# Kernel optimization log

Measured on AMD Instinct MI355X. Metric: run time of the kernel, lower is better.

The kernel has to match this reference:

```python
import jax, jax.numpy as jnp
import numpy as np

NHEADS = 16  # init kwarg


def setup_inputs() -> dict:
    key = jax.random.key(0)
    ks = jax.random.split(key, 3)
    S, B, E = 2048, 4, 1024
    x = jax.random.normal(ks[0], (S, B, E), dtype=jnp.float32)
    Wqkv = jax.random.normal(ks[1], (E, 3 * E), dtype=jnp.float32) * 0.02
    bqkv = jnp.zeros((3 * E,), dtype=jnp.float32)
    Wout = jax.random.normal(ks[2], (E, E), dtype=jnp.float32) * 0.02
    bout = jnp.zeros((E,), dtype=jnp.float32)
    return {"x": x, "Wqkv": Wqkv, "bqkv": bqkv, "Wout": Wout, "bout": bout}


def reference(x, Wqkv, bqkv, Wout, bout):
    S, B, E = x.shape
    H = NHEADS
    d = E // H
    scale = jnp.sqrt(jnp.asarray(E / H, dtype=x.dtype))  # sqrt(d_head)
    qkv = x @ Wqkv + bqkv                      # (S, B, 3E)
    q, k, v = jnp.split(qkv, 3, axis=-1)       # each (S, B, E)
    # (S, B, E) -> (S, B*H, d) -> (B*H, S, d), matching torch reshape+permute
    q = q.reshape(S, B * H, d).transpose(1, 0, 2)
    k = k.reshape(S, B * H, d).transpose(1, 0, 2)
    v = v.reshape(S, B * H, d).transpose(1, 0, 2)
    scores = jnp.einsum('hsd,htd->hst', q, k) / scale  # (B*H, S, S)
    attn = jax.nn.softmax(scores, axis=-1)
    o = jnp.einsum('hst,htd->hsd', attn, v)    # (B*H, S, d)
    o = o.transpose(1, 0, 2).reshape(S, B, E)  # back to (S, B, E)
    return o @ Wout + bout
```

## Files before the change

### kernel.cpp

```cpp
#include <hip/hip_runtime.h>

typedef short s16x8 __attribute__((ext_vector_type(8)));
typedef float f32x4 __attribute__((ext_vector_type(4)));
typedef float f32x16 __attribute__((ext_vector_type(16)));
typedef unsigned int u32x2 __attribute__((ext_vector_type(2)));

__device__ inline float bf2f(unsigned short u) {
    union { float f; unsigned int i; } x; x.i = ((unsigned int)u) << 16; return x.f;
}
__device__ inline unsigned short f2bf(float f) {
    union { float f; unsigned int i; } x; x.f = f;
    unsigned int r = x.i + 0x7fff + ((x.i >> 16) & 1);
    return (unsigned short)(r >> 16);
}
__device__ inline unsigned int pack_bf16(float a, float b) {
    unsigned int ia = __float_as_uint(a) + 0x8000u;
    unsigned int ib = __float_as_uint(b) + 0x8000u;
    return (ia >> 16) | (ib & 0xffff0000u);
}

__device__ inline void gload_lds16(const unsigned short* g, unsigned short* l) {
    __builtin_amdgcn_global_load_lds(
        (const __attribute__((address_space(1))) unsigned int*)g,
        (__attribute__((address_space(3))) unsigned int*)l, 16, 0, 0);
}

__global__ void detect_dtype(const unsigned short* __restrict__ x16, int* flag) {
    __shared__ int s[256];
    int tid = threadIdx.x;
    int cnt = 0;
    for (int i = tid; i < 4096; i += 256) {
        unsigned short u = x16[2 * i];
        int e = (u >> 7) & 0xFF;
        if (e >= 117 && e <= 129) cnt++;
    }
    s[tid] = cnt;
    __syncthreads();
    for (int off = 128; off; off >>= 1) {
        if (tid < off) s[tid] += s[tid + off];
        __syncthreads();
    }
    if (tid == 0) *flag = (s[0] < 2048) ? 1 : 0;
}

__global__ void convert_x(const void* __restrict__ in, unsigned short* __restrict__ out,
                          const int* __restrict__ flag, int n) {
    int mode = *flag;
    int i0 = (blockIdx.x * 256 + threadIdx.x) * 8;
    if (i0 >= n) return;
    if (mode) {
        const float* f = (const float*)in;
#pragma unroll
        for (int j = 0; j < 8; ++j) out[i0 + j] = f2bf(f[i0 + j]);
    } else {
        *(s16x8*)(out + i0) = *(const s16x8*)((const unsigned short*)in + i0);
    }
}

__global__ void cvt_bias(const void* __restrict__ in, float* __restrict__ out,
                         const int* __restrict__ flag, int n) {
    int i = blockIdx.x * 256 + threadIdx.x;
    if (i >= n) return;
    out[i] = (*flag) ? ((const float*)in)[i] : bf2f(((const unsigned short*)in)[i]);
}

__global__ void transpose_cvt(const void* __restrict__ in, unsigned short* __restrict__ out,
                              const int* __restrict__ flag, int R, int C) {
    __shared__ unsigned short t[64][72];
    int mode = *flag;
    int r0 = blockIdx.y * 64, c0 = blockIdx.x * 64;
    for (int i = threadIdx.x; i < 64 * 64; i += 256) {
        int r = i >> 6, c = i & 63;
        size_t idx = (size_t)(r0 + r) * C + (c0 + c);
        t[r][c] = mode ? f2bf(((const float*)in)[idx]) : ((const unsigned short*)in)[idx];
    }
    __syncthreads();
    for (int i = threadIdx.x; i < 64 * 64; i += 256) {
        int c = i >> 6, r = i & 63;
        out[(size_t)(c0 + c) * R + (r0 + r)] = t[r][c];
    }
}

__global__ __launch_bounds__(256) void transpose_v(
    const unsigned short* __restrict__ qkv, unsigned short* __restrict__ Vt) {
    __shared__ unsigned short t[64][72];
    int bh = blockIdx.y; int b = bh >> 4, h = bh & 15;
    int k0 = blockIdx.x * 64;
    int tid = threadIdx.x;
    int kr = tid >> 2, db = (tid & 3) * 16;
    const unsigned short* src = qkv + ((size_t)(k0 + kr) * 4 + b) * 3072 + 2048 + h * 64 + db;
    *(s16x8*)&t[kr][db] = *(const s16x8*)src;
    *(s16x8*)&t[kr][db + 8] = *(const s16x8*)(src + 8);
    __syncthreads();
    int d = tid >> 2, kb = (tid & 3) * 16;
    unsigned short* dst = Vt + (size_t)bh * 131072 + (size_t)d * 2048 + k0 + kb;
    s16x8 a, c;
#pragma unroll
    for (int j = 0; j < 8; ++j) a[j] = t[kb + j][d];
#pragma unroll
    for (int j = 0; j < 8; ++j) c[j] = t[kb + 8 + j][d];
    *(s16x8*)dst = a;
    *(s16x8*)(dst + 8) = c;
}

__global__ __launch_bounds__(512) void gemm_pipe_kernel(
    const unsigned short* __restrict__ A, const unsigned short* __restrict__ BT,
    const float* __restrict__ bias, void* __restrict__ Cout,
    int M, int N, int K, int qcols, float qscale, const int* __restrict__ outf32flag) {
    __shared__ unsigned short As[3][256 * 64];
    __shared__ unsigned short Bs[3][128 * 64];
    int tid = threadIdx.x;
    int lane = tid & 63, w = tid >> 6;
    int wr = w >> 1, wc = w & 1;
    int g = lane >> 4, qh = lane & 15;
    int m0 = blockIdx.y * 256, n0 = blockIdx.x * 128;
    int vxor = (lane & 7) ^ (lane >> 3);
    int axor = qh & 7;

    f32x4 z = {0.f, 0.f, 0.f, 0.f};
    f32x4 acc[4][4];
#pragma unroll
    for (int m = 0; m < 4; ++m)
#pragma unroll
        for (int n = 0; n < 4; ++n) acc[m][n] = z;

    const unsigned short* Asrc = A + (size_t)(m0 + w * 8 + (lane >> 3)) * K + vxor * 8;
    const unsigned short* Bsrc = BT + (size_t)(n0 + w * 8 + (lane >> 3)) * K + vxor * 8;

#define STAGE_A(buf, t, j) gload_lds16(Asrc + (size_t)(j) * 64 * K + (size_t)(t) * 64, \
                                       &As[buf][0] + (j) * 4096 + w * 512)
#define STAGE_B(buf, t, j) gload_lds16(Bsrc + (size_t)(j) * 64 * K + (size_t)(t) * 64, \
                                       &Bs[buf][0] + (j) * 4096 + w * 512)

    int NT = K >> 6;
    STAGE_A(0, 0, 0); STAGE_A(0, 0, 1); STAGE_A(0, 0, 2); STAGE_A(0, 0, 3);
    STAGE_B(0, 0, 0); STAGE_B(0, 0, 1);
    STAGE_A(1, 1, 0); STAGE_A(1, 1, 1); STAGE_A(1, 1, 2); STAGE_A(1, 1, 3);
    STAGE_B(1, 1, 0); STAGE_B(1, 1, 1);
    asm volatile("s_waitcnt vmcnt(6)" ::: "memory");
    __builtin_amdgcn_s_barrier();

    int cur = 0;
    for (int t = 0; t < NT; ++t) {
        int nx = cur + 2; if (nx >= 3) nx -= 3;
        bool pf = (t + 2) < NT;
        const unsigned short* Ab = &As[cur][0];
        const unsigned short* Bb = &Bs[cur][0];

        s16x8 bf[4][2];
#pragma unroll
        for (int n = 0; n < 4; ++n)
#pragma unroll
            for (int kk = 0; kk < 2; ++kk)
                bf[n][kk] = *(const s16x8*)(Bb + (size_t)(wc * 64 + n * 16 + qh) * 64 +
                                            (((kk * 4 + g) ^ axor) * 8));

        if (pf) { STAGE_A(nx, t + 2, 0); STAGE_A(nx, t + 2, 1); STAGE_B(nx, t + 2, 0); }
        {
            s16x8 af[2][2];
#pragma unroll
            for (int i = 0; i < 2; ++i)
#pragma unroll
                for (int kk = 0; kk < 2; ++kk)
                    af[i][kk] = *(const s16x8*)(Ab + (size_t)(wr * 64 + i * 16 + qh) * 64 +
                                                (((kk * 4 + g) ^ axor) * 8));
            __builtin_amdgcn_s_setprio(1);
#pragma unroll
            for (int kk = 0; kk < 2; ++kk)
#pragma unroll
                for (int i = 0; i < 2; ++i)
#pragma unroll
                    for (int n = 0; n < 4; ++n)
                        acc[i][n] = __builtin_amdgcn_mfma_f32_16x16x32_bf16(af[i][kk], bf[n][kk], acc[i][n], 0, 0, 0);
            __builtin_amdgcn_s_setprio(0);
        }
        __builtin_amdgcn_s_barrier();

        if (pf) { STAGE_A(nx, t + 2, 2); STAGE_A(nx, t + 2, 3); STAGE_B(nx, t + 2, 1); }
        {
            s16x8 af[2][2];
#pragma unroll
            for (int i = 0; i < 2; ++i)
#pragma unroll
                for (int kk = 0; kk < 2; ++kk)
                    af[i][kk] = *(const s16x8*)(Ab + (size_t)(wr * 64 + (i + 2) * 16 + qh) * 64 +
                                                (((kk * 4 + g) ^ axor) * 8));
            __builtin_amdgcn_s_setprio(1);
#pragma unroll
            for (int kk = 0; kk < 2; ++kk)
#pragma unroll
                for (int i = 0; i < 2; ++i)
#pragma unroll
                    for (int n = 0; n < 4; ++n)
                        acc[i + 2][n] = __builtin_amdgcn_mfma_f32_16x16x32_bf16(af[i][kk], bf[n][kk], acc[i + 2][n], 0, 0, 0);
            __builtin_amdgcn_s_setprio(0);
        }
        if (t + 1 < NT) {
            if (pf) asm volatile("s_waitcnt vmcnt(6)" ::: "memory");
            else    asm volatile("s_waitcnt vmcnt(0)" ::: "memory");
            __builtin_amdgcn_s_barrier();
        }
        cur = cur + 1; if (cur >= 3) cur -= 3;
    }
#undef STAGE_A
#undef STAGE_B

    bool f32out = (outf32flag != nullptr) && (*outf32flag != 0);
    int crow0 = m0 + wr * 64;
    int ccol0 = n0 + wc * 64;
#pragma unroll
    for (int n = 0; n < 4; ++n) {
        int col = ccol0 + n * 16 + qh;
        float bv = bias[col];
        float qs = (col < qcols) ? qscale : 1.0f;
#pragma unroll
        for (int m = 0; m < 4; ++m) {
            int rbase = crow0 + m * 16 + g * 4;
#pragma unroll
            for (int qq = 0; qq < 4; ++qq) {
                float v = (acc[m][n][qq] + bv) * qs;
                if (f32out)
                    ((float*)Cout)[(size_t)(rbase + qq) * N + col] = v;
                else
                    ((unsigned short*)Cout)[(size_t)(rbase + qq) * N + col] = f2bf(v);
            }
        }
    }
}

__global__ __launch_bounds__(256) void attn_kernel(
    const unsigned short* __restrict__ qkv, const unsigned short* __restrict__ Vt,
    unsigned short* __restrict__ O) {
    int bh = blockIdx.y;
    int b = bh >> 4, h = bh & 15;
    int q0 = blockIdx.x * 128;
    int tid = threadIdx.x, lane = tid & 63, w = tid >> 6;
    int l31 = lane & 31, l5 = lane >> 5;

    __shared__ unsigned short Ks[8 * 64 * 8];
    __shared__ unsigned short Vs[64 * 64];

    int qrow = q0 + w * 32 + l31;
    const unsigned short* qp = qkv + ((size_t)qrow * 4 + b) * 3072 + h * 64 + l5 * 8;
    s16x8 qf[4];
#pragma unroll
    for (int st = 0; st < 4; ++st) qf[st] = *(const s16x8*)(qp + st * 16);

    f32x16 z16 = {0.f,0.f,0.f,0.f,0.f,0.f,0.f,0.f,0.f,0.f,0.f,0.f,0.f,0.f,0.f,0.f};
    f32x16 oacc[2];
    oacc[0] = z16; oacc[1] = z16;
    float lrun = 0.f;

    int vxor = (lane & 7) ^ (lane >> 3);

    for (int k0 = 0; k0 < 2048; k0 += 64) {
        __syncthreads();
        {
            const unsigned short* ksrc = qkv + ((size_t)(k0 + lane) * 4 + b) * 3072 + 1024 + h * 64;
            gload_lds16(ksrc + w * 8, Ks + (size_t)w * 512);
            gload_lds16(ksrc + (w + 4) * 8, Ks + (size_t)(w + 4) * 512);
        }
#pragma unroll
        for (int c = 0; c < 2; ++c) {
            int d = (c * 4 + w) * 8 + (lane >> 3);
            const unsigned short* vsrc = Vt + (size_t)bh * 131072 + (size_t)d * 2048 + k0 + vxor * 8;
            gload_lds16(vsrc, Vs + (size_t)(c * 4 + w) * 512);
        }
        __syncthreads();

        f32x16 sc[2];
        sc[0] = z16; sc[1] = z16;
#pragma unroll
        for (int st = 0; st < 4; ++st) {
            int gd = st * 2 + l5;
#pragma unroll
            for (int kt = 0; kt < 2; ++kt) {
                s16x8 kf = *(const s16x8*)(Ks + ((size_t)(gd * 64 + kt * 32 + l31)) * 8);
                sc[kt] = __builtin_amdgcn_mfma_f32_32x32x16_bf16(kf, qf[st], sc[kt], 0, 0, 0);
            }
        }

        float rsum = 0.f;
#pragma unroll
        for (int kt = 0; kt < 2; ++kt) {
            float p[16];
#pragma unroll
            for (int r = 0; r < 16; ++r) {
                p[r] = __builtin_amdgcn_exp2f(sc[kt][r]);
                rsum += p[r];
            }
#pragma unroll
            for (int ks1 = 0; ks1 < 2; ++ks1) {
                unsigned int A0 = pack_bf16(p[8 * ks1 + 0], p[8 * ks1 + 1]);
                unsigned int A1 = pack_bf16(p[8 * ks1 + 2], p[8 * ks1 + 3]);
                unsigned int B0 = pack_bf16(p[8 * ks1 + 4], p[8 * ks1 + 5]);
                unsigned int B1 = pack_bf16(p[8 * ks1 + 6], p[8 * ks1 + 7]);
                u32x2 r0 = __builtin_amdgcn_permlane32_swap(A0, B0, false, false);
                u32x2 r1 = __builtin_amdgcn_permlane32_swap(A1, B1, false, false);
                union { unsigned int u[4]; s16x8 v; } uu;
                uu.u[0] = r0[0];
                uu.u[1] = r1[0];
                uu.u[2] = r0[1];
                uu.u[3] = r1[1];
                int ks = kt * 2 + ks1;
#pragma unroll
                for (int dt = 0; dt < 2; ++dt) {
                    int d = dt * 32 + l31;
                    int kb = (ks * 2 + l5) ^ (d & 7);
                    s16x8 vf = *(const s16x8*)(Vs + (size_t)d * 64 + kb * 8);
                    oacc[dt] = __builtin_amdgcn_mfma_f32_32x32x16_bf16(vf, uu.v, oacc[dt], 0, 0, 0);
                }
            }
        }
        rsum += __shfl_xor(rsum, 32);
        lrun += rsum;
    }

    float rl = 1.f / lrun;
    unsigned short* orow = O + ((size_t)qrow * 4 + b) * 1024 + h * 64 + l5 * 4;
#pragma unroll
    for (int dt = 0; dt < 2; ++dt) {
#pragma unroll
        for (int g2 = 0; g2 < 4; ++g2) {
            u32x2 pv;
            pv[0] = pack_bf16(oacc[dt][4 * g2 + 0] * rl, oacc[dt][4 * g2 + 1] * rl);
            pv[1] = pack_bf16(oacc[dt][4 * g2 + 2] * rl, oacc[dt][4 * g2 + 3] * rl);
            *(u32x2*)(orow + dt * 32 + g2 * 8) = pv;
        }
    }
}

extern "C" void kernel_launch(void* const* d_in, const int* in_sizes, int n_in,
                              void* d_out, int out_size, void* d_ws, size_t ws_size,
                              hipStream_t stream) {
    const void* x    = d_in[0];
    const void* Wqkv = d_in[1];
    const void* bqkv = d_in[2];
    const void* Wout = d_in[3];
    const void* bout = d_in[4];

    char* ws = (char*)d_ws;
    unsigned short* qkv   = (unsigned short*)(ws);
    unsigned short* Obuf  = (unsigned short*)(ws + 50331648);
    unsigned short* WqkvT = (unsigned short*)(ws + 67108864);
    unsigned short* WoutT = (unsigned short*)(ws + 73400320);
    unsigned short* xb    = (unsigned short*)(ws + 75497472);
    unsigned short* Vtg   = xb;
    float*          bq_f  = (float*)(ws + 92274688);
    float*          bo_f  = (float*)(ws + 92286976);
    int*            flag  = (int*)(ws + 92291072);

    detect_dtype<<<1, 256, 0, stream>>>((const unsigned short*)x, flag);
    convert_x<<<4096, 256, 0, stream>>>(x, xb, flag, 8388608);
    cvt_bias<<<12, 256, 0, stream>>>(bqkv, bq_f, flag, 3072);
    cvt_bias<<<4, 256, 0, stream>>>(bout, bo_f, flag, 1024);
    transpose_cvt<<<dim3(48, 16), 256, 0, stream>>>(Wqkv, WqkvT, flag, 1024, 3072);
    transpose_cvt<<<dim3(16, 16), 256, 0, stream>>>(Wout, WoutT, flag, 1024, 1024);

    gemm_pipe_kernel<<<dim3(24, 32), 512, 0, stream>>>(xb, WqkvT, bq_f, qkv,
                                                       8192, 3072, 1024, 1024, 0.18033688f, nullptr);
    transpose_v<<<dim3(32, 64), 256, 0, stream>>>(qkv, Vtg);
    attn_kernel<<<dim3(16, 64), 256, 0, stream>>>(qkv, Vtg, Obuf);
    gemm_pipe_kernel<<<dim3(8, 32), 512, 0, stream>>>(Obuf, WoutT, bo_f, d_out,
                                                      8192, 1024, 1024, 0, 1.0f, flag);
}
```

Before: 282.8 us.

## Remap attention blocks per XCD, hoist K/V pointers, vectorize bf16 conversion

Attention blocks are remapped so the eight batch-heads sharing an XCD id are handled by blocks dispatched to the same XCD, which is meant to improve L2 reuse of K/V tiles. Per-iteration K and V address computation is replaced by pointers that are incremented each tile. The fp32 to bf16 input conversion now uses 128-bit loads and stores, and pack_bf16 uses a single byte-permute instruction. The remap assumes round-robin XCD dispatch and a grid of exactly 16x64 blocks.

```diff
diff --git a/kernel.cpp b/kernel.cpp
--- a/kernel.cpp
+++ b/kernel.cpp
@@ -4,6 +4,7 @@
 typedef float f32x4 __attribute__((ext_vector_type(4)));
 typedef float f32x16 __attribute__((ext_vector_type(16)));
 typedef unsigned int u32x2 __attribute__((ext_vector_type(2)));
+typedef unsigned int u32x4 __attribute__((ext_vector_type(4)));
 
 __device__ inline float bf2f(unsigned short u) {
     union { float f; unsigned int i; } x; x.i = ((unsigned int)u) << 16; return x.f;
@@ -16,7 +17,7 @@
 __device__ inline unsigned int pack_bf16(float a, float b) {
     unsigned int ia = __float_as_uint(a) + 0x8000u;
     unsigned int ib = __float_as_uint(b) + 0x8000u;
-    return (ia >> 16) | (ib & 0xffff0000u);
+    return __builtin_amdgcn_perm(ib, ia, 0x07060302u);
 }
 
 __device__ inline void gload_lds16(const unsigned short* g, unsigned short* l) {
@@ -49,9 +50,15 @@
     int i0 = (blockIdx.x * 256 + threadIdx.x) * 8;
     if (i0 >= n) return;
     if (mode) {
-        const float* f = (const float*)in;
-#pragma unroll
-        for (int j = 0; j < 8; ++j) out[i0 + j] = f2bf(f[i0 + j]);
+        const f32x4* f = (const f32x4*)in;
+        f32x4 a = f[i0 >> 2];
+        f32x4 c = f[(i0 >> 2) + 1];
+        u32x4 o;
+        o[0] = pack_bf16(a[0], a[1]);
+        o[1] = pack_bf16(a[2], a[3]);
+        o[2] = pack_bf16(c[0], c[1]);
+        o[3] = pack_bf16(c[2], c[3]);
+        *(u32x4*)(out + i0) = o;
     } else {
         *(s16x8*)(out + i0) = *(const s16x8*)((const unsigned short*)in + i0);
     }
@@ -231,9 +238,12 @@
 __global__ __launch_bounds__(256) void attn_kernel(
     const unsigned short* __restrict__ qkv, const unsigned short* __restrict__ Vt,
     unsigned short* __restrict__ O) {
-    int bh = blockIdx.y;
+    int L = blockIdx.y * 16 + blockIdx.x;
+    int xcd = L & 7;
+    int i = L >> 3;
+    int bh = xcd * 8 + (i & 7);
+    int q0 = (i >> 3) << 7;
     int b = bh >> 4, h = bh & 15;
-    int q0 = blockIdx.x * 128;
     int tid = threadIdx.x, lane = tid & 63, w = tid >> 6;
     int l31 = lane & 31, l5 = lane >> 5;
 
@@ -253,19 +263,21 @@
 
     int vxor = (lane & 7) ^ (lane >> 3);
 
-    for (int k0 = 0; k0 < 2048; k0 += 64) {
+    const unsigned short* kptr = qkv + ((size_t)lane * 4 + b) * 3072 + 1024 + h * 64;
+    const unsigned short* vp0 = Vt + (size_t)bh * 131072 +
+                                (size_t)((0 * 4 + w) * 8 + (lane >> 3)) * 2048 + vxor * 8;
+    const unsigned short* vp1 = Vt + (size_t)bh * 131072 +
+                                (size_t)((1 * 4 + w) * 8 + (lane >> 3)) * 2048 + vxor * 8;
+
+    for (int t = 0; t < 32; ++t) {
         __syncthreads();
-        {
-            const unsigned short* ksrc = qkv + ((size_t)(k0 + lane) * 4 + b) * 3072 + 1024 + h * 64;
-            gload_lds16(ksrc + w * 8, Ks + (size_t)w * 512);
-            gload_lds16(ksrc + (w + 4) * 8, Ks + (size_t)(w + 4) * 512);
-        }
-#pragma unroll
-        for (int c = 0; c < 2; ++c) {
-            int d = (c * 4 + w) * 8 + (lane >> 3);
-            const unsigned short* vsrc = Vt + (size_t)bh * 131072 + (size_t)d * 2048 + k0 + vxor * 8;
-            gload_lds16(vsrc, Vs + (size_t)(c * 4 + w) * 512);
-        }
+        gload_lds16(kptr + w * 8, Ks + (size_t)w * 512);
+        gload_lds16(kptr + (w + 4) * 8, Ks + (size_t)(w + 4) * 512);
+        gload_lds16(vp0, Vs + (size_t)w * 512);
+        gload_lds16(vp1, Vs + (size_t)(4 + w) * 512);
+        kptr += 786432;
+        vp0 += 64;
+        vp1 += 64;
         __syncthreads();
 
         f32x16 sc[2];
```

Result: no change. 282.0 us (-0.3%).
